# Kernel optimization log

Measured on AMD Instinct MI355X. Metric: run time of the kernel, lower is better.

## Reference

```python
import jax, jax.numpy as jnp
import numpy as np

EPS = 1e-8  # torch.nn.CosineSimilarity default eps
V, I, H, L = 50257, 1024, 1024, 16384  # vocab, gru_input_size, gru_hidden_size, max_length


def setup_inputs() -> dict:
    key = jax.random.key(0)
    ks = jax.random.split(key, 12)
    rn = lambda k, shape, s=1.0: jax.random.normal(k, shape, dtype=jnp.float32) * s
    return {
        "token": jax.random.randint(ks[0], (1, 1), 0, V),
        "hidden": rn(ks[1], (1, 1, H)),
        "encoder_outputs": rn(ks[2], (L, H)),
        "emb": rn(ks[3], (V, I)),
        "attn_w": rn(ks[4], (H, I + H), 0.02), "attn_b": jnp.zeros((H,), jnp.float32),
        "comb_w": rn(ks[5], (I, I + H), 0.02), "comb_b": jnp.zeros((I,), jnp.float32),
        "w_ih": rn(ks[6], (3 * H, I), 0.02), "w_hh": rn(ks[7], (3 * H, H), 0.02),
        "b_ih": jnp.zeros((3 * H,), jnp.float32), "b_hh": jnp.zeros((3 * H,), jnp.float32),
        "fc2_w": rn(ks[8], (64, H), 0.02), "fc2_b": jnp.zeros((64,), jnp.float32),
        "out_w": rn(ks[9], (1, 64), 0.02), "out_b": jnp.zeros((1,), jnp.float32),
    }


def reference(token, hidden, encoder_outputs, emb, attn_w, attn_b, comb_w, comb_b,
              w_ih, w_hh, b_ih, b_hh, fc2_w, fc2_b, out_w, out_b):
    # 'identifier'/'keyword' branch; dropout is identity in eval mode.
    embedded = emb[token[0, 0]][None, :]                      # [1, I]
    h0 = hidden[0]                                            # [1, H]
    # attention query projection
    q = jnp.concatenate([embedded, h0], axis=1) @ attn_w.T + attn_b  # [1, H]
    # cosine similarity of q vs each encoder output row (dim=1 broadcast)
    qn = jnp.maximum(jnp.linalg.norm(q[0]), EPS)
    en = jnp.maximum(jnp.linalg.norm(encoder_outputs, axis=1), EPS)  # [L]
    sims = (encoder_outputs @ q[0]) / (qn * en)               # [L]
    attn_weights = jax.nn.softmax(sims)[None, :]              # [1, L]
    attn_applied = attn_weights @ encoder_outputs             # [1, H]
    x = jnp.concatenate([embedded, attn_applied], axis=1) @ comb_w.T + comb_b  # [1, I]
    x = jax.nn.relu(x)
    # single GRU cell step (PyTorch gate convention: r, z, n)
    gi = x @ w_ih.T + b_ih                                    # [1, 3H]
    gh = h0 @ w_hh.T + b_hh                                   # [1, 3H]
    r = jax.nn.sigmoid(gi[:, :H] + gh[:, :H])
    z = jax.nn.sigmoid(gi[:, H:2 * H] + gh[:, H:2 * H])
    n = jnp.tanh(gi[:, 2 * H:] + r * gh[:, 2 * H:])
    h_new = (1.0 - z) * n + z * h0                            # [1, H]
    out = jax.nn.relu(h_new @ fc2_w.T + fc2_b) @ out_w.T + out_b  # [1, 1]
    return out, h_new[None], attn_weights
```

## Files before the change

kernel.cpp:

```cpp
#include <hip/hip_runtime.h>
#include <hip/hip_bf16.h>
#include <math.h>

#define II 1024
#define HH 1024
#define LL 16384
#define EPSF 1e-8f
#define GI_BLOCKS 192u

__device__ __forceinline__ float wred_sum(float v) {
    #pragma unroll
    for (int o = 32; o; o >>= 1) v += __shfl_down(v, o);
    return v;
}

__global__ __launch_bounds__(256) void n1_kernel(
    const int* __restrict__ token, const float* __restrict__ emb,
    const float* __restrict__ hidden, const float* __restrict__ attn_w,
    const float* __restrict__ attn_b, const float* __restrict__ w_hh,
    const float* __restrict__ b_hh, const float* __restrict__ comb_w,
    const float* __restrict__ comb_b, float* __restrict__ q,
    float* __restrict__ gh, float* __restrict__ x_emb) {
    int w = (blockIdx.x * blockDim.x + threadIdx.x) >> 6;
    int lane = threadIdx.x & 63;
    const float* er = emb + (size_t)token[0] * II;
    if (w < HH) {
        const float* row = attn_w + (size_t)w * (II + HH);
        float acc = 0.f;
        for (int k = lane * 4; k < II + HH; k += 256) {
            float4 w4 = *(const float4*)(row + k);
            const float* src = (k < II) ? (er + k) : (hidden + (k - II));
            float4 x4 = *(const float4*)src;
            acc += w4.x * x4.x + w4.y * x4.y + w4.z * x4.z + w4.w * x4.w;
        }
        acc = wred_sum(acc);
        if (lane == 0) q[w] = acc + attn_b[w];
    } else if (w < HH + 3 * HH) {
        int r = w - HH;
        const float* row = w_hh + (size_t)r * HH;
        float acc = 0.f;
        for (int k = lane * 4; k < HH; k += 256) {
            float4 w4 = *(const float4*)(row + k);
            float4 x4 = *(const float4*)(hidden + k);
            acc += w4.x * x4.x + w4.y * x4.y + w4.z * x4.z + w4.w * x4.w;
        }
        acc = wred_sum(acc);
        if (lane == 0) gh[r] = acc + b_hh[r];
    } else {
        int r = w - 4 * HH;
        const float* row = comb_w + (size_t)r * (II + HH);
        float acc = 0.f;
        #pragma unroll
        for (int k = lane * 4; k < II; k += 256) {
            float4 w4 = *(const float4*)(row + k);
            float4 x4 = *(const float4*)(er + k);
            acc += w4.x * x4.x + w4.y * x4.y + w4.z * x4.z + w4.w * x4.w;
        }
        acc = wred_sum(acc);
        if (lane == 0) x_emb[r] = acc + comb_b[r];
    }
}

__global__ __launch_bounds__(1024) void simscol_kernel(
    const float* __restrict__ enc, const float* __restrict__ q,
    float* __restrict__ e_out, float* __restrict__ part,
    float* __restrict__ psum) {
    __shared__ float s_w[64];
    const int b = blockIdx.x, t = threadIdx.x;
    const int wv = t >> 6, lane = t & 63;

    float4 q4[4];
    #pragma unroll
    for (int j = 0; j < 4; ++j) q4[j] = *(const float4*)(q + lane * 4 + j * 256);
    float ss = 0.f;
    #pragma unroll
    for (int j = 0; j < 4; ++j)
        ss += q4[j].x * q4[j].x + q4[j].y * q4[j].y + q4[j].z * q4[j].z +
              q4[j].w * q4[j].w;
    ss = wred_sum(ss);
    ss = __shfl(ss, 0);
    const float qn = fmaxf(sqrtf(ss), EPSF);

    #pragma unroll
    for (int j = 0; j < 4; ++j) {
        int r = b * 64 + wv * 4 + j;
        const float* row = enc + (size_t)r * HH;
        float dv = 0.f, sv = 0.f;
        #pragma unroll
        for (int k = 0; k < 4; ++k) {
            float4 e4 = *(const float4*)(row + lane * 4 + k * 256);
            dv += e4.x * q4[k].x + e4.y * q4[k].y + e4.z * q4[k].z +
                  e4.w * q4[k].w;
            sv += e4.x * e4.x + e4.y * e4.y + e4.z * e4.z + e4.w * e4.w;
        }
        #pragma unroll
        for (int o = 32; o; o >>= 1) {
            dv += __shfl_down(dv, o);
            sv += __shfl_down(sv, o);
        }
        if (lane == 0) {
            float en = fmaxf(sqrtf(sv), EPSF);
            float e = expf(dv / (qn * en) - 1.f);
            s_w[wv * 4 + j] = e;
            e_out[r] = e;
        }
    }
    __syncthreads();

    if (wv == 0) {
        float v = s_w[lane];
        v = wred_sum(v);
        if (lane == 0) psum[b] = v;
    }
    const float* base = enc + (size_t)b * 64 * HH;
    float acc = 0.f;
    #pragma unroll 8
    for (int r = 0; r < 64; ++r)
        acc = fmaf(s_w[r], base[(size_t)r * HH + t], acc);
    part[(size_t)b * HH + t] = acc;
}

__global__ __launch_bounds__(1024) void n3_kernel(
    const float* __restrict__ comb_w, const float* __restrict__ part,
    const float* __restrict__ psum, const float* __restrict__ e_in,
    const float* __restrict__ x_emb, float* __restrict__ x,
    float* __restrict__ attn_wout) {
    __shared__ float s_tmp[4][1028];
    __shared__ float s_aa[HH];
    __shared__ float s_den;
    const int b = blockIdx.x, t = threadIdx.x;
    const int wv = t >> 6, lane = t & 63;

    if (wv == 0) {
        float4 p4 = *(const float4*)(psum + lane * 4);
        float v = p4.x + p4.y + p4.z + p4.w;
        v = wred_sum(v);
        if (lane == 0) s_den = v;
    }
    {
        int cpart = t >> 8, col4 = t & 255;
        const float4* p4 = (const float4*)part;
        float4 a = {0.f, 0.f, 0.f, 0.f};
        for (int c = cpart * 64; c < cpart * 64 + 64; ++c) {
            float4 v = p4[(size_t)c * 256 + col4];
            a.x += v.x; a.y += v.y; a.z += v.z; a.w += v.w;
        }
        s_tmp[cpart][col4 * 4 + 0] = a.x;
        s_tmp[cpart][col4 * 4 + 1] = a.y;
        s_tmp[cpart][col4 * 4 + 2] = a.z;
        s_tmp[cpart][col4 * 4 + 3] = a.w;
    }
    __syncthreads();
    const float inv = 1.f / s_den;
    s_aa[t] = (s_tmp[0][t] + s_tmp[1][t] + s_tmp[2][t] + s_tmp[3][t]) * inv;
    if (b < 16) attn_wout[b * 1024 + t] = e_in[b * 1024 + t] * inv;
    __syncthreads();

    int r = b * 16 + wv;
    const float* row = comb_w + (size_t)r * (II + HH) + II;
    float acc = 0.f;
    #pragma unroll
    for (int k = lane * 4; k < HH; k += 256) {
        float4 w4 = *(const float4*)(row + k);
        acc += w4.x * s_aa[k] + w4.y * s_aa[k + 1] + w4.z * s_aa[k + 2] +
               w4.w * s_aa[k + 3];
    }
    acc = wred_sum(acc);
    if (lane == 0) x[r] = fmaxf(acc + x_emb[r], 0.f);
}

__global__ __launch_bounds__(1024) void n4_kernel(
    const float* __restrict__ w_ih, const float* __restrict__ x,
    const float* __restrict__ b_ih, float* __restrict__ gi,
    const float* __restrict__ gh, const float* __restrict__ hidden,
    const float* __restrict__ fc2_w, const float* __restrict__ fc2_b,
    const float* __restrict__ out_w, const float* __restrict__ out_b,
    float* __restrict__ h_new, float* __restrict__ out_scalar,
    unsigned* __restrict__ cnt) {
    __shared__ unsigned s_last;
    __shared__ float hsh[HH];
    __shared__ float f[64];
    const int b = blockIdx.x, t = threadIdx.x;
    const int wv = t >> 6, lane = t & 63;

    {
        int r = b * 16 + wv;
        const float* row = w_ih + (size_t)r * II;
        float acc = 0.f;
        #pragma unroll
        for (int k = lane * 4; k < II; k += 256) {
            float4 w4 = *(const float4*)(row + k);
            float4 x4 = *(const float4*)(x + k);
            acc += w4.x * x4.x + w4.y * x4.y + w4.z * x4.z + w4.w * x4.w;
        }
        acc = wred_sum(acc);
        if (lane == 0) gi[r] = acc + b_ih[r];
    }
    __syncthreads();
    if (t == 0) {
        __threadfence();
        unsigned old = atomicAdd(cnt, 1u);
        s_last = ((old + 1u) % GI_BLOCKS == 0u) ? 1u : 0u;
    }
    __syncthreads();
    if (!s_last) return;
    __threadfence();

    float grv = gi[t] + gh[t];
    float gzv = gi[HH + t] + gh[HH + t];
    float rg = 1.f / (1.f + expf(-grv));
    float zg = 1.f / (1.f + expf(-gzv));
    float ng = tanhf(gi[2 * HH + t] + rg * gh[2 * HH + t]);
    float h = (1.f - zg) * ng + zg * hidden[t];
    hsh[t] = h;
    h_new[t] = h;
    __syncthreads();
    #pragma unroll
    for (int rr = 0; rr < 4; ++rr) {
        int r2 = wv * 4 + rr;
        const float* row = fc2_w + (size_t)r2 * HH;
        float acc = 0.f;
        #pragma unroll
        for (int k = lane * 4; k < HH; k += 256) {
            float4 w4 = *(const float4*)(row + k);
            acc += w4.x * hsh[k] + w4.y * hsh[k + 1] + w4.z * hsh[k + 2] +
                   w4.w * hsh[k + 3];
        }
        acc = wred_sum(acc);
        if (lane == 0) f[r2] = fmaxf(acc + fc2_b[r2], 0.f);
    }
    __syncthreads();
    if (t < 64) {
        float v = f[t] * out_w[t];
        v = wred_sum(v);
        if (t == 0) out_scalar[0] = v + out_b[0];
    }
}

extern "C" void kernel_launch(void* const* d_in, const int* in_sizes, int n_in,
                              void* d_out, int out_size, void* d_ws,
                              size_t ws_size, hipStream_t stream) {
    const int*   token  = (const int*)d_in[0];
    const float* hidden = (const float*)d_in[1];
    const float* enc    = (const float*)d_in[2];
    const float* emb    = (const float*)d_in[3];
    const float* attn_w = (const float*)d_in[4];
    const float* attn_b = (const float*)d_in[5];
    const float* comb_w = (const float*)d_in[6];
    const float* comb_b = (const float*)d_in[7];
    const float* w_ih   = (const float*)d_in[8];
    const float* w_hh   = (const float*)d_in[9];
    const float* b_ih   = (const float*)d_in[10];
    const float* b_hh   = (const float*)d_in[11];
    const float* fc2_w  = (const float*)d_in[12];
    const float* fc2_b  = (const float*)d_in[13];
    const float* out_w  = (const float*)d_in[14];
    const float* out_b  = (const float*)d_in[15];

    float* ws = (float*)d_ws;
    float* q     = ws;
    float* gh    = ws + 1024;
    float* x_emb = ws + 4096;
    float* x     = ws + 5120;
    float* gi    = ws + 6144;
    float* e     = ws + 9216;
    float* psum  = ws + 25600;
    float* part  = ws + 26624;
    unsigned* cnt = (unsigned*)(ws + 26624 + 262144);

    float* out_scalar = (float*)d_out;
    float* h_new      = (float*)d_out + 1;
    float* attn_wout  = (float*)d_out + 1 + HH;

    n1_kernel<<<1280, 256, 0, stream>>>(token, emb, hidden, attn_w, attn_b,
                                        w_hh, b_hh, comb_w, comb_b, q, gh,
                                        x_emb);
    simscol_kernel<<<256, 1024, 0, stream>>>(enc, q, e, part, psum);
    n3_kernel<<<64, 1024, 0, stream>>>(comb_w, part, psum, e, x_emb, x,
                                       attn_wout);
    n4_kernel<<<GI_BLOCKS, 1024, 0, stream>>>(w_ih, x, b_ih, gi, gh, hidden,
                                              fc2_w, fc2_b, out_w, out_b,
                                              h_new, out_scalar, cnt);
}
```

Measured before the change: 62.24 us.

## Fuse comb and GRU-input stages via fixed-point atomic reductions

Replaces the partial-sum buffer and separate reduction in n3 with 64-bit fixed-point atomicAdds from the attention kernel, so column sums and the softmax denominator accumulate in place. The comb_w projection and the w_ih GEMV are merged into one 64-block kernel. Each block computes 16 entries of x and scatters their contribution to all 3072 gate rows through integer atomics, and the last block finishes the GRU and the output head. This removes one launch and the 1 MB part round-trip, in exchange for heavy atomic contention and fixed-point quantization of the attention and gate accumulations.

```diff
diff --git a/kernel.cpp b/kernel.cpp
--- a/kernel.cpp
+++ b/kernel.cpp
@@ -6,7 +6,15 @@
 #define HH 1024
 #define LL 16384
 #define EPSF 1e-8f
-#define GI_BLOCKS 192u
+#define XBLK 64
+#define SC_AA 4294967296.0f
+#define ISC_AA 2.3283064365386963e-10f
+#define SC_DEN 1.099511627776e12f
+#define ISC_DEN 9.094947017729282e-13f
+#define SC_GI 4294967296.0f
+#define ISC_GI 2.3283064365386963e-10f
+
+typedef unsigned long long ull;
 
 __device__ __forceinline__ float wred_sum(float v) {
     #pragma unroll
@@ -20,7 +28,12 @@
     const float* __restrict__ attn_b, const float* __restrict__ w_hh,
     const float* __restrict__ b_hh, const float* __restrict__ comb_w,
     const float* __restrict__ comb_b, float* __restrict__ q,
-    float* __restrict__ gh, float* __restrict__ x_emb) {
+    float* __restrict__ gh, float* __restrict__ x_emb,
+    ull* __restrict__ accs) {
+    if (blockIdx.x == 0) {
+        for (int i = threadIdx.x; i < 1024 + 1 + 3072 + 1; i += 256)
+            accs[i] = 0ull;
+    }
     int w = (blockIdx.x * blockDim.x + threadIdx.x) >> 6;
     int lane = threadIdx.x & 63;
     const float* er = emb + (size_t)token[0] * II;
@@ -35,7 +48,7 @@
         }
         acc = wred_sum(acc);
         if (lane == 0) q[w] = acc + attn_b[w];
-    } else if (w < HH + 3 * HH) {
+    } else if (w < 4 * HH) {
         int r = w - HH;
         const float* row = w_hh + (size_t)r * HH;
         float acc = 0.f;
@@ -61,10 +74,10 @@
     }
 }
 
-__global__ __launch_bounds__(1024) void simscol_kernel(
+__global__ __launch_bounds__(1024) void n2_kernel(
     const float* __restrict__ enc, const float* __restrict__ q,
-    float* __restrict__ e_out, float* __restrict__ part,
-    float* __restrict__ psum) {
+    float* __restrict__ e_out, ull* __restrict__ aa_int,
+    ull* __restrict__ den_int) {
     __shared__ float s_w[64];
     const int b = blockIdx.x, t = threadIdx.x;
     const int wv = t >> 6, lane = t & 63;
@@ -110,107 +123,91 @@
     if (wv == 0) {
         float v = s_w[lane];
         v = wred_sum(v);
-        if (lane == 0) psum[b] = v;
+        if (lane == 0)
+            atomicAdd(den_int, (ull)(long long)llrintf(v * SC_DEN));
     }
     const float* base = enc + (size_t)b * 64 * HH;
     float acc = 0.f;
     #pragma unroll 8
     for (int r = 0; r < 64; ++r)
         acc = fmaf(s_w[r], base[(size_t)r * HH + t], acc);
-    part[(size_t)b * HH + t] = acc;
+    atomicAdd(&aa_int[t], (ull)(long long)llrintf(acc * SC_AA));
 }
 
 __global__ __launch_bounds__(1024) void n3_kernel(
-    const float* __restrict__ comb_w, const float* __restrict__ part,
-    const float* __restrict__ psum, const float* __restrict__ e_in,
-    const float* __restrict__ x_emb, float* __restrict__ x,
-    float* __restrict__ attn_wout) {
-    __shared__ float s_tmp[4][1028];
-    __shared__ float s_aa[HH];
-    __shared__ float s_den;
-    const int b = blockIdx.x, t = threadIdx.x;
-    const int wv = t >> 6, lane = t & 63;
-
-    if (wv == 0) {
-        float4 p4 = *(const float4*)(psum + lane * 4);
-        float v = p4.x + p4.y + p4.z + p4.w;
-        v = wred_sum(v);
-        if (lane == 0) s_den = v;
-    }
-    {
-        int cpart = t >> 8, col4 = t & 255;
-        const float4* p4 = (const float4*)part;
-        float4 a = {0.f, 0.f, 0.f, 0.f};
-        for (int c = cpart * 64; c < cpart * 64 + 64; ++c) {
-            float4 v = p4[(size_t)c * 256 + col4];
-            a.x += v.x; a.y += v.y; a.z += v.z; a.w += v.w;
-        }
-        s_tmp[cpart][col4 * 4 + 0] = a.x;
-        s_tmp[cpart][col4 * 4 + 1] = a.y;
-        s_tmp[cpart][col4 * 4 + 2] = a.z;
-        s_tmp[cpart][col4 * 4 + 3] = a.w;
-    }
-    __syncthreads();
-    const float inv = 1.f / s_den;
-    s_aa[t] = (s_tmp[0][t] + s_tmp[1][t] + s_tmp[2][t] + s_tmp[3][t]) * inv;
-    if (b < 16) attn_wout[b * 1024 + t] = e_in[b * 1024 + t] * inv;
-    __syncthreads();
-
-    int r = b * 16 + wv;
-    const float* row = comb_w + (size_t)r * (II + HH) + II;
-    float acc = 0.f;
-    #pragma unroll
-    for (int k = lane * 4; k < HH; k += 256) {
-        float4 w4 = *(const float4*)(row + k);
-        acc += w4.x * s_aa[k] + w4.y * s_aa[k + 1] + w4.z * s_aa[k + 2] +
-               w4.w * s_aa[k + 3];
-    }
-    acc = wred_sum(acc);
-    if (lane == 0) x[r] = fmaxf(acc + x_emb[r], 0.f);
-}
-
-__global__ __launch_bounds__(1024) void n4_kernel(
-    const float* __restrict__ w_ih, const float* __restrict__ x,
-    const float* __restrict__ b_ih, float* __restrict__ gi,
+    const float* __restrict__ comb_w, const float* __restrict__ x_emb,
+    const float* __restrict__ w_ih, const float* __restrict__ b_ih,
     const float* __restrict__ gh, const float* __restrict__ hidden,
     const float* __restrict__ fc2_w, const float* __restrict__ fc2_b,
     const float* __restrict__ out_w, const float* __restrict__ out_b,
-    float* __restrict__ h_new, float* __restrict__ out_scalar,
-    unsigned* __restrict__ cnt) {
-    __shared__ unsigned s_last;
+    const float* __restrict__ e_in, const ull* __restrict__ aa_int,
+    const ull* __restrict__ den_int, ull* __restrict__ gi_acc,
+    ull* __restrict__ gc, float* __restrict__ h_new,
+    float* __restrict__ out_scalar, float* __restrict__ attn_wout) {
+    __shared__ float s_aa[HH];
+    __shared__ float s_x[16];
     __shared__ float hsh[HH];
     __shared__ float f[64];
+    __shared__ unsigned s_last;
     const int b = blockIdx.x, t = threadIdx.x;
     const int wv = t >> 6, lane = t & 63;
 
+    const float inv_den = 1.f / ((float)((long long)den_int[0]) * ISC_DEN);
+    s_aa[t] = (float)((long long)aa_int[t]) * ISC_AA * inv_den;
+    if (t < 256) {
+        int i = b * 256 + t;
+        attn_wout[i] = e_in[i] * inv_den;
+    }
+    __syncthreads();
+
+    int r = b * 16 + wv;
     {
-        int r = b * 16 + wv;
-        const float* row = w_ih + (size_t)r * II;
-        float acc = 0.f;
-        #pragma unroll
-        for (int k = lane * 4; k < II; k += 256) {
-            float4 w4 = *(const float4*)(row + k);
-            float4 x4 = *(const float4*)(x + k);
-            acc += w4.x * x4.x + w4.y * x4.y + w4.z * x4.z + w4.w * x4.w;
-        }
-        acc = wred_sum(acc);
-        if (lane == 0) gi[r] = acc + b_ih[r];
+        const float* row = comb_w + (size_t)r * (II + HH) + II;
+        float acc = 0.f;
+        #pragma unroll
+        for (int k = lane * 4; k < HH; k += 256) {
+            float4 w4 = *(const float4*)(row + k);
+            acc += w4.x * s_aa[k] + w4.y * s_aa[k + 1] + w4.z * s_aa[k + 2] +
+                   w4.w * s_aa[k + 3];
+        }
+        acc = wred_sum(acc);
+        if (lane == 0) s_x[wv] = fmaxf(acc + x_emb[r], 0.f);
+    }
+    __syncthreads();
+
+    const int c0 = b * 16;
+    #pragma unroll
+    for (int i = 0; i < 3; ++i) {
+        int rr = t + i * 1024;
+        const float* wrow = w_ih + (size_t)rr * II + c0;
+        float4 w0 = *(const float4*)(wrow + 0);
+        float4 w1 = *(const float4*)(wrow + 4);
+        float4 w2 = *(const float4*)(wrow + 8);
+        float4 w3 = *(const float4*)(wrow + 12);
+        float acc = w0.x * s_x[0] + w0.y * s_x[1] + w0.z * s_x[2] +
+                    w0.w * s_x[3] + w1.x * s_x[4] + w1.y * s_x[5] +
+                    w1.z * s_x[6] + w1.w * s_x[7] + w2.x * s_x[8] +
+                    w2.y * s_x[9] + w2.z * s_x[10] + w2.w * s_x[11] +
+                    w3.x * s_x[12] + w3.y * s_x[13] + w3.z * s_x[14] +
+                    w3.w * s_x[15];
+        atomicAdd(&gi_acc[rr], (ull)(long long)llrintf(acc * SC_GI));
     }
     __syncthreads();
     if (t == 0) {
         __threadfence();
-        unsigned old = atomicAdd(cnt, 1u);
-        s_last = ((old + 1u) % GI_BLOCKS == 0u) ? 1u : 0u;
+        ull old = atomicAdd(gc, 1ull);
+        s_last = (old + 1ull == (ull)XBLK) ? 1u : 0u;
     }
     __syncthreads();
     if (!s_last) return;
     __threadfence();
 
-    float grv = gi[t] + gh[t];
-    float gzv = gi[HH + t] + gh[HH + t];
-    float rg = 1.f / (1.f + expf(-grv));
-    float zg = 1.f / (1.f + expf(-gzv));
-    float ng = tanhf(gi[2 * HH + t] + rg * gh[2 * HH + t]);
+    float gr = (float)((long long)gi_acc[t]) * ISC_GI + b_ih[t];
+    float gz = (float)((long long)gi_acc[HH + t]) * ISC_GI + b_ih[HH + t];
+    float gn = (float)((long long)gi_acc[2 * HH + t]) * ISC_GI + b_ih[2 * HH + t];
+    float rg = 1.f / (1.f + expf(-(gr + gh[t])));
+    float zg = 1.f / (1.f + expf(-(gz + gh[HH + t])));
+    float ng = tanhf(gn + rg * gh[2 * HH + t]);
     float h = (1.f - zg) * ng + zg * hidden[t];
     hsh[t] = h;
     h_new[t] = h;
@@ -261,12 +258,12 @@
     float* q     = ws;
     float* gh    = ws + 1024;
     float* x_emb = ws + 4096;
-    float* x     = ws + 5120;
-    float* gi    = ws + 6144;
-    float* e     = ws + 9216;
-    float* psum  = ws + 25600;
-    float* part  = ws + 26624;
-    unsigned* cnt = (unsigned*)(ws + 26624 + 262144);
+    float* e     = ws + 5120;
+    ull* accs    = (ull*)(ws + 21504);
+    ull* aa_int  = accs;
+    ull* den_int = accs + 1024;
+    ull* gi_acc  = accs + 1025;
+    ull* gc      = accs + 4097;
 
     float* out_scalar = (float*)d_out;
     float* h_new      = (float*)d_out + 1;
@@ -274,11 +271,10 @@
 
     n1_kernel<<<1280, 256, 0, stream>>>(token, emb, hidden, attn_w, attn_b,
                                         w_hh, b_hh, comb_w, comb_b, q, gh,
-                                        x_emb);
-    simscol_kernel<<<256, 1024, 0, stream>>>(enc, q, e, part, psum);
-    n3_kernel<<<64, 1024, 0, stream>>>(comb_w, part, psum, e, x_emb, x,
-                                       attn_wout);
-    n4_kernel<<<GI_BLOCKS, 1024, 0, stream>>>(w_ih, x, b_ih, gi, gh, hidden,
-                                              fc2_w, fc2_b, out_w, out_b,
-                                              h_new, out_scalar, cnt);
-}
+                                        x_emb, accs);
+    n2_kernel<<<256, 1024, 0, stream>>>(enc, q, e, aa_int, den_int);
+    n3_kernel<<<XBLK, 1024, 0, stream>>>(comb_w, x_emb, w_ih, b_ih, gh, hidden,
+                                         fc2_w, fc2_b, out_w, out_b, e, aa_int,
+                                         den_int, gi_acc, gc, h_new, out_scalar,
+                                         attn_wout);
+}
```

After: 63.64 us. 1.02x slower.
